# Optimization experiments

Hardware: AMD Instinct MI355X
Metric: run time of the kernel (lower is better)

## Reference

```python
import jax, jax.numpy as jnp
import numpy as np

DIM = 768
NUM_HEADS = 12
WH, WW = 14, 14
N_TOK = WH * WW + 1  # 197, includes CLS token
NUM_REL_DIST = (2 * WH - 1) * (2 * WW - 1) + 3  # 732
HEAD_DIM = DIM // NUM_HEADS
SCALE = HEAD_DIM ** -0.5


def _relative_position_index():
    # Mirrors the torch buffer construction (constant, int).
    coords = np.stack(np.meshgrid(np.arange(WH), np.arange(WW), indexing='ij'))  # [2,WH,WW]
    cf = coords.reshape(2, -1)  # [2, WH*WW]
    rel = cf[:, :, None] - cf[:, None, :]  # [2, N, N]
    rel = rel.transpose(1, 2, 0).astype(np.int64)
    rel[:, :, 0] += WH - 1
    rel[:, :, 1] += WW - 1
    rel[:, :, 0] *= 2 * WW - 1
    idx = np.zeros((N_TOK, N_TOK), dtype=np.int64)
    idx[1:, 1:] = rel.sum(-1)
    idx[0, 0:] = NUM_REL_DIST - 3
    idx[0:, 0] = NUM_REL_DIST - 2
    idx[0, 0] = NUM_REL_DIST - 1
    return jnp.asarray(idx)

REL_POS_INDEX = _relative_position_index()


def setup_inputs() -> dict:
    key = jax.random.key(0)
    ks = jax.random.split(key, 7)
    B = 64
    x = jax.random.normal(ks[0], (B, N_TOK, DIM), dtype=jnp.float32)
    qkv_weight = jax.random.normal(ks[1], (3 * DIM, DIM), dtype=jnp.float32) * 0.02
    q_bias = jax.random.normal(ks[2], (DIM,), dtype=jnp.float32) * 0.02
    v_bias = jax.random.normal(ks[3], (DIM,), dtype=jnp.float32) * 0.02
    rel_pos_bias_table = jax.random.normal(ks[4], (NUM_REL_DIST, NUM_HEADS), dtype=jnp.float32) * 0.02
    proj_weight = jax.random.normal(ks[5], (DIM, DIM), dtype=jnp.float32) * 0.02
    proj_bias = jax.random.normal(ks[6], (DIM,), dtype=jnp.float32) * 0.02
    return {"x": x, "qkv_weight": qkv_weight, "q_bias": q_bias, "v_bias": v_bias,
            "rel_pos_bias_table": rel_pos_bias_table, "proj_weight": proj_weight,
            "proj_bias": proj_bias}


def reference(x, qkv_weight, q_bias, v_bias, rel_pos_bias_table, proj_weight, proj_bias):
    B, N, C = x.shape
    qkv_bias = jnp.concatenate([q_bias, jnp.zeros_like(v_bias), v_bias])
    qkv = x @ qkv_weight.T + qkv_bias  # [B, N, 3C]
    qkv = qkv.reshape(B, N, 3, NUM_HEADS, HEAD_DIM).transpose(2, 0, 3, 1, 4)
    q, k, v = qkv[0], qkv[1], qkv[2]  # each [B, H, N, D]
    attn = jnp.einsum('bhnd,bhmd->bhnm', q * SCALE, k)  # [B, H, N, N]
    rpb = rel_pos_bias_table[REL_POS_INDEX]  # [N, N, H]
    attn = attn + rpb.transpose(2, 0, 1)[None]  # [1, H, N, N]
    attn = jax.nn.softmax(attn, axis=-1)
    out = jnp.einsum('bhnm,bhmd->bhnd', attn, v)  # [B, H, N, D]
    out = out.transpose(0, 2, 1, 3).reshape(B, N, C)
    return out @ proj_weight.T + proj_bias
```

## Files before the change

### kernel.cpp

```cpp
#include <hip/hip_runtime.h>
#include <hip/hip_bf16.h>

#define DIM 768
#define QKVD 2304
#define NHEADS 12
#define NTOK 197
#define NP 208
#define NPS 232
#define M_ROWS 12608
#define M_PAD 12800
#define HEADS_TOT 768
#define NT 24

typedef __attribute__((ext_vector_type(8))) short bf16x8;
typedef __attribute__((ext_vector_type(4))) float f32x4;

__device__ inline short f2bf(float f) {
  union { __hip_bfloat16 h; short s; } u;
  u.h = __float2bfloat16(f);
  return u.s;
}

__device__ __forceinline__ void gload16(const short* g, short* l) {
  __builtin_amdgcn_global_load_lds((const __attribute__((address_space(1))) void*)g,
                                   (__attribute__((address_space(3))) void*)l, 16, 0, 0);
}

__device__ __forceinline__ int xcd_swz(int orig, int nwg) {
  int q = nwg >> 3, r = nwg & 7;
  int x = orig & 7, p = orig >> 3;
  return (x < r ? x * (q + 1) : r * (q + 1) + (x - r) * q) + p;
}

__global__ void prep_kernel(const float* __restrict__ x, const float* __restrict__ wq,
                            const float* __restrict__ wp, const float* __restrict__ table,
                            short* __restrict__ xb, short* __restrict__ wqb,
                            short* __restrict__ wpb, float* __restrict__ rpbf) {
  int idx = blockIdx.x * 256 + threadIdx.x;
  const int n_x  = M_ROWS * DIM / 4;
  const int n_wq = 3 * DIM * DIM / 4;
  const int n_wp = DIM * DIM / 4;
  const int n_pad = (M_PAD - M_ROWS) * DIM / 4;
  const int conv_tot = n_x + n_wq + n_wp + n_pad;
  if (idx < conv_tot) {
    if (idx >= n_x + n_wq + n_wp) {
      int k = idx - n_x - n_wq - n_wp;
      short4 z = {0, 0, 0, 0};
      *(short4*)(xb + (size_t)M_ROWS * DIM + (size_t)k * 4) = z;
      return;
    }
    const float4* src; short* dst; int off;
    if (idx < n_x)             { src = (const float4*)x;  dst = xb;  off = idx; }
    else if (idx < n_x + n_wq) { src = (const float4*)wq; dst = wqb; off = idx - n_x; }
    else                       { src = (const float4*)wp; dst = wpb; off = idx - n_x - n_wq; }
    float4 v = src[off];
    short4 o;
    o.x = f2bf(v.x); o.y = f2bf(v.y); o.z = f2bf(v.z); o.w = f2bf(v.w);
    *(short4*)(dst + (size_t)off * 4) = o;
    return;
  }
  int ridx = idx - conv_tot;
  if (ridx >= NHEADS * NP * NP) return;
  int h = ridx / (NP * NP);
  int rem = ridx - h * NP * NP;
  int i = rem / NP;
  int j = rem - i * NP;
  float v = 0.f;
  if (i < NTOK && j < NTOK) {
    int t;
    if (i == 0 && j == 0) t = 731;
    else if (i == 0)      t = 729;
    else if (j == 0)      t = 730;
    else {
      int p = i - 1, q = j - 1;
      int ri = p / 14, ci = p - ri * 14;
      int rj = q / 14, cj = q - rj * 14;
      t = (ri - rj + 13) * 27 + (ci - cj + 13);
    }
    v = table[t * NHEADS + h];
  }
  rpbf[ridx] = v;
}

__device__ __forceinline__ void tile_step(int kt, short* lds,
                                          const short* Asrc, const short* Bsrc, short* sdst,
                                          int aoff, int boff,
                                          bf16x8 (&afc)[8], bf16x8 (&bfc)[4],
                                          bf16x8 (&afn)[8], bf16x8 (&bfn)[4],
                                          f32x4 (&acc)[8][4]) {
  const bool stg = (kt < NT - 3);
  const bool pre = (kt < NT - 1);
  const short* nb = lds + ((kt + 1) & 3) * 16384;
  short* stgd = sdst + ((kt + 3) & 3) * 16384;
  const int kc = (kt + 3) * 32;
  if (stg) { gload16(Asrc + kc, stgd); gload16(Bsrc + kc, stgd + 8192); }
  if (pre) {
#pragma unroll
    for (int n = 0; n < 4; ++n) bfn[n] = *(const bf16x8*)(nb + boff + n * 512);
#pragma unroll
    for (int j = 0; j < 4; ++j) afn[j] = *(const bf16x8*)(nb + aoff + j * 512);
  }
  __builtin_amdgcn_s_setprio(1);
#pragma unroll
  for (int j = 0; j < 4; ++j)
#pragma unroll
    for (int n = 0; n < 4; ++n)
      acc[j][n] = __builtin_amdgcn_mfma_f32_16x16x32_bf16(afc[j], bfc[n], acc[j][n], 0, 0, 0);
  __builtin_amdgcn_s_setprio(0);
  if (stg) { gload16(Asrc + (size_t)128 * DIM + kc, stgd + 4096);
             gload16(Bsrc + (size_t)128 * DIM + kc, stgd + 8192 + 4096); }
  if (pre) {
#pragma unroll
    for (int j = 0; j < 4; ++j) afn[4 + j] = *(const bf16x8*)(nb + aoff + 2048 + j * 512);
  }
  __builtin_amdgcn_s_setprio(1);
#pragma unroll
  for (int j = 0; j < 4; ++j)
#pragma unroll
    for (int n = 0; n < 4; ++n)
      acc[4 + j][n] = __builtin_amdgcn_mfma_f32_16x16x32_bf16(afc[4 + j], bfc[n], acc[4 + j][n], 0, 0, 0);
  __builtin_amdgcn_s_setprio(0);
  if (kt < NT - 3)       { asm volatile("s_waitcnt vmcnt(4)" ::: "memory"); }
  else if (kt == NT - 3) { asm volatile("s_waitcnt vmcnt(0)" ::: "memory"); }
  __builtin_amdgcn_s_barrier();
}

__device__ __forceinline__ void gemm256_mainloop(const short* __restrict__ A,
                                                 const short* __restrict__ Bw,
                                                 int tm, int tn, short* lds, f32x4 (&acc)[8][4]) {
  const int tid = threadIdx.x;
  const int srow = tid >> 2;
  const int sslot = ((tid & 3) - (tid >> 3)) & 3;
  const int l = tid & 63, lr = l & 15, lg = l >> 4;
  const int w = tid >> 6, wm = w >> 2, wn = w & 3;
  const short* Asrc = A + (size_t)(tm * 256 + srow) * DIM + sslot * 8;
  const short* Bsrc = Bw + (size_t)(tn * 256 + srow) * DIM + sslot * 8;
  short* sdst = lds + tid * 8;
  const int slotR = (lg + (lr >> 1)) & 3;
  const int aoff = wm * 4096 + lr * 32 + slotR * 8;
  const int boff = 8192 + (wn >> 1) * 4096 + ((wn & 1) * 64 + lr) * 32 + slotR * 8;
#pragma unroll
  for (int m = 0; m < 8; ++m)
#pragma unroll
    for (int n = 0; n < 4; ++n) { f32x4 z = {0.f, 0.f, 0.f, 0.f}; acc[m][n] = z; }

#pragma unroll
  for (int kt = 0; kt < 3; ++kt) {
    gload16(Asrc + kt * 32, sdst + kt * 16384);
    gload16(Bsrc + kt * 32, sdst + kt * 16384 + 8192);
    gload16(Asrc + (size_t)128 * DIM + kt * 32, sdst + kt * 16384 + 4096);
    gload16(Bsrc + (size_t)128 * DIM + kt * 32, sdst + kt * 16384 + 8192 + 4096);
  }
  asm volatile("s_waitcnt vmcnt(4)" ::: "memory");
  __builtin_amdgcn_s_barrier();

  bf16x8 afA[8], bfA[4], afB[8], bfB[4];
#pragma unroll
  for (int n = 0; n < 4; ++n) bfA[n] = *(const bf16x8*)(lds + boff + n * 512);
#pragma unroll
  for (int j = 0; j < 4; ++j) afA[j] = *(const bf16x8*)(lds + aoff + j * 512);
#pragma unroll
  for (int j = 0; j < 4; ++j) afA[4 + j] = *(const bf16x8*)(lds + aoff + 2048 + j * 512);

  for (int kt = 0; kt < NT; kt += 2) {
    tile_step(kt,     lds, Asrc, Bsrc, sdst, aoff, boff, afA, bfA, afB, bfB, acc);
    tile_step(kt + 1, lds, Asrc, Bsrc, sdst, aoff, boff, afB, bfB, afA, bfA, acc);
  }
}

__global__ __launch_bounds__(512, 2)
void gemm_qkv_kernel(const short* __restrict__ xb, const short* __restrict__ wqb,
                     const float* __restrict__ q_bias, const float* __restrict__ v_bias,
                     short* __restrict__ qkvb) {
  __shared__ __attribute__((aligned(16))) short lds[65536];
  const int wg = xcd_swz(blockIdx.x, 50 * 9);
  const int tn = wg % 9, tm = wg / 9;
  f32x4 acc[8][4];
  gemm256_mainloop(xb, wqb, tm, tn, lds, acc);

  const int tid = threadIdx.x;
  const int w = tid >> 6, wm = w >> 2, wn = w & 3;
  const int l = tid & 63, lr = l & 15, lg = l >> 4;
  const int cbase = tn * 256 + wn * 64;
  for (int half = 0; half < 2; ++half) {
    if (wm == half) {
#pragma unroll
      for (int n = 0; n < 4; ++n) {
        int c = cbase + n * 16 + lr;
        int part = (c < 768) ? 0 : ((c < 1536) ? 1 : 2);
        float bias = (part == 0) ? q_bias[c] : ((part == 2) ? v_bias[c - 1536] : 0.f);
        float scl = (part == 0) ? 0.125f : 1.f;
#pragma unroll
        for (int m = 0; m < 8; ++m)
#pragma unroll
          for (int i = 0; i < 4; ++i)
            lds[(m * 16 + lg * 4 + i) * 264 + wn * 64 + n * 16 + lr] =
                f2bf((acc[m][n][i] + bias) * scl);
      }
    }
    __syncthreads();
#pragma unroll
    for (int p = 0; p < 8; ++p) {
      int chunk = tid + p * 512;
      int row = chunk >> 5, ch = chunk & 31;
      bf16x8 v = *(const bf16x8*)(lds + row * 264 + ch * 8);
      *(bf16x8*)(qkvb + (size_t)(tm * 256 + half * 128 + row) * QKVD + tn * 256 + ch * 8) = v;
    }
    __syncthreads();
  }
}

__device__ __forceinline__ void tile_step128(int kt, short* lds,
                                             const short* Asrc, const short* Bsrc, short* sdst,
                                             int aoff, int boff,
                                             bf16x8 (&afc)[4], bf16x8 (&bfc)[4],
                                             bf16x8 (&afn)[4], bf16x8 (&bfn)[4],
                                             f32x4 (&acc)[4][4]) {
  const bool stg = (kt < NT - 3);
  const bool pre = (kt < NT - 1);
  const short* nb = lds + ((kt + 1) & 3) * 8192;
  short* stgd = sdst + ((kt + 3) & 3) * 8192;
  const int kc = (kt + 3) * 32;
  if (stg) { gload16(Asrc + kc, stgd); gload16(Bsrc + kc, stgd + 4096); }
  if (pre) {
#pragma unroll
    for (int n = 0; n < 4; ++n) bfn[n] = *(const bf16x8*)(nb + boff + n * 512);
#pragma unroll
    for (int j = 0; j < 2; ++j) afn[j] = *(const bf16x8*)(nb + aoff + j * 512);
  }
  __builtin_amdgcn_s_setprio(1);
#pragma unroll
  for (int j = 0; j < 2; ++j)
#pragma unroll
    for (int n = 0; n < 4; ++n)
      acc[j][n] = __builtin_amdgcn_mfma_f32_16x16x32_bf16(afc[j], bfc[n], acc[j][n], 0, 0, 0);
  __builtin_amdgcn_s_setprio(0);
  if (stg) { gload16(Asrc + (size_t)64 * DIM + kc, stgd + 2048);
             gload16(Bsrc + (size_t)64 * DIM + kc, stgd + 4096 + 2048); }
  if (pre) {
#pragma unroll
    for (int j = 2; j < 4; ++j) afn[j] = *(const bf16x8*)(nb + aoff + j * 512);
  }
  __builtin_amdgcn_s_setprio(1);
#pragma unroll
  for (int j = 2; j < 4; ++j)
#pragma unroll
    for (int n = 0; n < 4; ++n)
      acc[j][n] = __builtin_amdgcn_mfma_f32_16x16x32_bf16(afc[j], bfc[n], acc[j][n], 0, 0, 0);
  __builtin_amdgcn_s_setprio(0);
  if (kt < NT - 3)       { asm volatile("s_waitcnt vmcnt(4)" ::: "memory"); }
  else if (kt == NT - 3) { asm volatile("s_waitcnt vmcnt(0)" ::: "memory"); }
  __builtin_amdgcn_s_barrier();
}

__global__ __launch_bounds__(256, 2)
void gemm_proj_kernel(const short* __restrict__ ab, const short* __restrict__ wpb,
                      const float* __restrict__ proj_bias, float* __restrict__ out) {
  __shared__ __attribute__((aligned(16))) short lds[32768];
  const int wg = xcd_swz(blockIdx.x, 99 * 6);
  const int tn = wg % 6, tm = wg / 6;
  const int tid = threadIdx.x;
  const int srow = tid >> 2;
  const int sslot = ((tid & 3) - (tid >> 3)) & 3;
  const int l = tid & 63, lr = l & 15, lg = l >> 4;
  const int w = tid >> 6, wm = w >> 1, wn = w & 1;
  const short* Asrc = ab + (size_t)(tm * 128 + srow) * DIM + sslot * 8;
  const short* Bsrc = wpb + (size_t)(tn * 128 + srow) * DIM + sslot * 8;
  short* sdst = lds + tid * 8;
  const int slotR = (lg + (lr >> 1)) & 3;
  const int aoff = wm * 2048 + lr * 32 + slotR * 8;
  const int boff = 4096 + wn * 2048 + lr * 32 + slotR * 8;
  f32x4 acc[4][4];
#pragma unroll
  for (int m = 0; m < 4; ++m)
#pragma unroll
    for (int n = 0; n < 4; ++n) { f32x4 z = {0.f, 0.f, 0.f, 0.f}; acc[m][n] = z; }

#pragma unroll
  for (int kt = 0; kt < 3; ++kt) {
    gload16(Asrc + kt * 32, sdst + kt * 8192);
    gload16(Bsrc + kt * 32, sdst + kt * 8192 + 4096);
    gload16(Asrc + (size_t)64 * DIM + kt * 32, sdst + kt * 8192 + 2048);
    gload16(Bsrc + (size_t)64 * DIM + kt * 32, sdst + kt * 8192 + 4096 + 2048);
  }
  asm volatile("s_waitcnt vmcnt(4)" ::: "memory");
  __builtin_amdgcn_s_barrier();

  bf16x8 afA[4], bfA[4], afB[4], bfB[4];
#pragma unroll
  for (int n = 0; n < 4; ++n) bfA[n] = *(const bf16x8*)(lds + boff + n * 512);
#pragma unroll
  for (int j = 0; j < 4; ++j) afA[j] = *(const bf16x8*)(lds + aoff + j * 512);

  for (int kt = 0; kt < NT; kt += 2) {
    tile_step128(kt,     lds, Asrc, Bsrc, sdst, aoff, boff, afA, bfA, afB, bfB, acc);
    tile_step128(kt + 1, lds, Asrc, Bsrc, sdst, aoff, boff, afB, bfB, afA, bfA, acc);
  }

  float* ldsF = (float*)lds;
  for (int half = 0; half < 2; ++half) {
    if (wm == half) {
#pragma unroll
      for (int n = 0; n < 4; ++n) {
        int c = tn * 128 + wn * 64 + n * 16 + lr;
        float pb = proj_bias[c];
#pragma unroll
        for (int m = 0; m < 4; ++m)
#pragma unroll
          for (int i = 0; i < 4; ++i)
            ldsF[(m * 16 + lg * 4 + i) * 132 + wn * 64 + n * 16 + lr] = acc[m][n][i] + pb;
      }
    }
    __syncthreads();
#pragma unroll
    for (int p = 0; p < 8; ++p) {
      int chunk = tid + p * 256;
      int row = chunk >> 5, ch = chunk & 31;
      int r = tm * 128 + half * 64 + row;
      if (r < M_ROWS) {
        f32x4 v = *(const f32x4*)(ldsF + row * 132 + ch * 4);
        *(f32x4*)(out + (size_t)r * DIM + tn * 128 + ch * 4) = v;
      }
    }
    __syncthreads();
  }
}

__global__ __launch_bounds__(512, 1)
void attn_kernel(const short* __restrict__ qkvb, const float* __restrict__ rpbf,
                 short* __restrict__ aout) {
  __shared__ __attribute__((aligned(16))) short Klds[208 * 64];
  __shared__ __attribute__((aligned(16))) short Vlds[64 * NPS];
  __shared__ __attribute__((aligned(16))) short Plds[8 * 16 * NPS];
  const int bh = blockIdx.x;
  const int b = bh / 12, h = bh - b * 12;
  const short* base = qkvb + (size_t)(b * 197) * QKVD;
  const short* Qg = base + h * 64;
  const short* Kg = base + 768 + h * 64;
  const short* Vg = base + 1536 + h * 64;
  const float* RP = rpbf + (size_t)h * NP * NP;
  const int tid = threadIdx.x;
  const int wave = tid >> 6, l = tid & 63, lr = l & 15, lg = l >> 4;

  for (int c = tid; c < 1664; c += 512) {
    int r = c >> 3, sp = c & 7;
    int rr = r < NTOK ? r : NTOK - 1;
    gload16(Kg + (size_t)rr * QKVD + ((sp ^ (r & 7)) << 3), Klds + c * 8);
  }
  for (int idx = tid; idx < 64 * NP; idx += 512) {
    int t = idx >> 6, d = idx & 63;
    int tt = t < NTOK ? t : NTOK - 1;
    Vlds[d * NPS + t] = Vg[(size_t)tt * QKVD + d];
  }
  __syncthreads();
  if (tid < 64) {
    for (int j = NP; j < NPS; ++j) Vlds[tid * NPS + j] = 0;
  }
  __syncthreads();

  short* Pw = Plds + wave * 16 * NPS;
  for (int s = wave; s < 13; s += 8) {
    const int row0 = s * 16;
    const int qrow = (row0 + lr < NTOK) ? (row0 + lr) : (NTOK - 1);
    bf16x8 qf0 = *(const bf16x8*)(Qg + (size_t)qrow * QKVD + lg * 8);
    bf16x8 qf1 = *(const bf16x8*)(Qg + (size_t)qrow * QKVD + 32 + lg * 8);
    f32x4 acc[13];
#pragma unroll
    for (int t = 0; t < 13; ++t) { f32x4 z = {0.f, 0.f, 0.f, 0.f}; acc[t] = z; }
    __builtin_amdgcn_s_setprio(1);
#pragma unroll
    for (int t = 0; t < 13; ++t) {
      int rk = t * 16 + lr;
      int sw = lr & 7;
      bf16x8 kf0 = *(const bf16x8*)(Klds + rk * 64 + ((lg ^ sw) << 3));
      bf16x8 kf1 = *(const bf16x8*)(Klds + rk * 64 + (((4 + lg) ^ sw) << 3));
      acc[t] = __builtin_amdgcn_mfma_f32_16x16x32_bf16(qf0, kf0, acc[t], 0, 0, 0);
      acc[t] = __builtin_amdgcn_mfma_f32_16x16x32_bf16(qf1, kf1, acc[t], 0, 0, 0);
    }
    __builtin_amdgcn_s_setprio(0);
    float sum4[4];
#pragma unroll
    for (int i = 0; i < 4; ++i) {
      const int row = row0 + lg * 4 + i;
      const float* rp = RP + (size_t)row * NP;
      float sv[13];
      float mx = -3e38f;
#pragma unroll
      for (int t = 0; t < 13; ++t) {
        int col = t * 16 + lr;
        float s_ = (col < NTOK) ? (acc[t][i] + rp[col]) : -3e38f;
        sv[t] = s_;
        mx = fmaxf(mx, s_);
      }
      mx = fmaxf(mx, __shfl_xor(mx, 1, 16));
      mx = fmaxf(mx, __shfl_xor(mx, 2, 16));
      mx = fmaxf(mx, __shfl_xor(mx, 4, 16));
      mx = fmaxf(mx, __shfl_xor(mx, 8, 16));
      float sm = 0.f;
#pragma unroll
      for (int t = 0; t < 13; ++t) {
        float p = __expf(sv[t] - mx);
        sm += p;
        Pw[(lg * 4 + i) * NPS + t * 16 + lr] = f2bf(p);
      }
      sm += __shfl_xor(sm, 1, 16);
      sm += __shfl_xor(sm, 2, 16);
      sm += __shfl_xor(sm, 4, 16);
      sm += __shfl_xor(sm, 8, 16);
      sum4[i] = sm;
      Pw[(lg * 4 + i) * NPS + 208 + lr] = 0;
    }
    f32x4 o[4];
#pragma unroll
    for (int dt = 0; dt < 4; ++dt) { f32x4 z = {0.f, 0.f, 0.f, 0.f}; o[dt] = z; }
    __builtin_amdgcn_s_setprio(1);
#pragma unroll
    for (int jb = 0; jb < 7; ++jb) {
      bf16x8 pf = *(const bf16x8*)(Pw + lr * NPS + jb * 32 + lg * 8);
#pragma unroll
      for (int dt = 0; dt < 4; ++dt) {
        bf16x8 vf = *(const bf16x8*)(Vlds + (dt * 16 + lr) * NPS + jb * 32 + lg * 8);
        o[dt] = __builtin_amdgcn_mfma_f32_16x16x32_bf16(pf, vf, o[dt], 0, 0, 0);
      }
    }
    __builtin_amdgcn_s_setprio(0);
#pragma unroll
    for (int i = 0; i < 4; ++i) {
      const int row = row0 + lg * 4 + i;
      if (row < NTOK) {
        float inv = 1.f / sum4[i];
        size_t base2 = (size_t)(b * 197 + row) * DIM + h * 64;
#pragma unroll
        for (int dt = 0; dt < 4; ++dt)
          aout[base2 + dt * 16 + lr] = f2bf(o[dt][i] * inv);
      }
    }
  }
}

extern "C" void kernel_launch(void* const* d_in, const int* in_sizes, int n_in,
                              void* d_out, int out_size, void* d_ws, size_t ws_size,
                              hipStream_t stream) {
  const float* x         = (const float*)d_in[0];
  const float* wqkv      = (const float*)d_in[1];
  const float* q_bias    = (const float*)d_in[2];
  const float* v_bias    = (const float*)d_in[3];
  const float* table     = (const float*)d_in[4];
  const float* wproj     = (const float*)d_in[5];
  const float* proj_bias = (const float*)d_in[6];
  float* out = (float*)d_out;

  char* p = (char*)d_ws;
  short* xb    = (short*)p; p += (size_t)M_PAD * DIM * 2;
  short* wqb   = (short*)p; p += (size_t)3 * DIM * DIM * 2;
  short* wpb   = (short*)p; p += (size_t)DIM * DIM * 2;
  short* qkvb  = (short*)p; p += (size_t)M_PAD * QKVD * 2;
  float* rpbf  = (float*)p; p += (size_t)NHEADS * NP * NP * 4;
  short* aout  = xb;

  const int conv_tot = (M_ROWS * DIM + 3 * DIM * DIM + DIM * DIM + (M_PAD - M_ROWS) * DIM) / 4;
  const int prep_tot = conv_tot + NHEADS * NP * NP;
  prep_kernel<<<(prep_tot + 255) / 256, 256, 0, stream>>>(x, wqkv, wproj, table, xb, wqb, wpb, rpbf);
  gemm_qkv_kernel<<<50 * 9, 512, 0, stream>>>(xb, wqb, q_bias, v_bias, qkvb);
  attn_kernel<<<HEADS_TOT, 512, 0, stream>>>(qkvb, rpbf, aout);
  gemm_proj_kernel<<<99 * 6, 256, 0, stream>>>(aout, wpb, proj_bias, out);
}
```

Measured before the change: 141.6 us.

## Shrink attention blocks to 256 threads with two per CU and compact LDS

```diff
diff --git a/kernel.cpp b/kernel.cpp
--- a/kernel.cpp
+++ b/kernel.cpp
@@ -6,7 +6,8 @@
 #define NHEADS 12
 #define NTOK 197
 #define NP 208
-#define NPS 232
+#define VST 208
+#define PST 216
 #define M_ROWS 12608
 #define M_PAD 12800
 #define HEADS_TOT 768
@@ -326,12 +327,12 @@
   }
 }
 
-__global__ __launch_bounds__(512, 1)
+__global__ __launch_bounds__(256, 2)
 void attn_kernel(const short* __restrict__ qkvb, const float* __restrict__ rpbf,
                  short* __restrict__ aout) {
   __shared__ __attribute__((aligned(16))) short Klds[208 * 64];
-  __shared__ __attribute__((aligned(16))) short Vlds[64 * NPS];
-  __shared__ __attribute__((aligned(16))) short Plds[8 * 16 * NPS];
+  __shared__ __attribute__((aligned(16))) short Vlds[64 * VST];
+  __shared__ __attribute__((aligned(16))) short Plds[4 * 16 * PST];
   const int bh = blockIdx.x;
   const int b = bh / 12, h = bh - b * 12;
   const short* base = qkvb + (size_t)(b * 197) * QKVD;
@@ -342,24 +343,24 @@
   const int tid = threadIdx.x;
   const int wave = tid >> 6, l = tid & 63, lr = l & 15, lg = l >> 4;
 
-  for (int c = tid; c < 1664; c += 512) {
+  for (int c = tid; c < 1664; c += 256) {
     int r = c >> 3, sp = c & 7;
     int rr = r < NTOK ? r : NTOK - 1;
     gload16(Kg + (size_t)rr * QKVD + ((sp ^ (r & 7)) << 3), Klds + c * 8);
   }
-  for (int idx = tid; idx < 64 * NP; idx += 512) {
-    int t = idx >> 6, d = idx & 63;
+  for (int vi = tid; vi < 1664; vi += 256) {
+    int t = vi >> 3, j = vi & 7;
     int tt = t < NTOK ? t : NTOK - 1;
-    Vlds[d * NPS + t] = Vg[(size_t)tt * QKVD + d];
+    bf16x8 v = *(const bf16x8*)(Vg + (size_t)tt * QKVD + j * 8);
+    int ts = t ^ ((j & 1) << 3);
+#pragma unroll
+    for (int e = 0; e < 8; ++e)
+      Vlds[(j * 8 + e) * VST + ts] = v[e];
   }
   __syncthreads();
-  if (tid < 64) {
-    for (int j = NP; j < NPS; ++j) Vlds[tid * NPS + j] = 0;
-  }
-  __syncthreads();
-
-  short* Pw = Plds + wave * 16 * NPS;
-  for (int s = wave; s < 13; s += 8) {
+
+  short* Pw = Plds + wave * 16 * PST;
+  for (int s = wave; s < 13; s += 4) {
     const int row0 = s * 16;
     const int qrow = (row0 + lr < NTOK) ? (row0 + lr) : (NTOK - 1);
     bf16x8 qf0 = *(const bf16x8*)(Qg + (size_t)qrow * QKVD + lg * 8);
@@ -401,26 +402,37 @@
       for (int t = 0; t < 13; ++t) {
         float p = __expf(sv[t] - mx);
         sm += p;
-        Pw[(lg * 4 + i) * NPS + t * 16 + lr] = f2bf(p);
+        Pw[(lg * 4 + i) * PST + t * 16 + lr] = f2bf(p);
       }
       sm += __shfl_xor(sm, 1, 16);
       sm += __shfl_xor(sm, 2, 16);
       sm += __shfl_xor(sm, 4, 16);
       sm += __shfl_xor(sm, 8, 16);
       sum4[i] = sm;
-      Pw[(lg * 4 + i) * NPS + 208 + lr] = 0;
     }
     f32x4 o[4];
 #pragma unroll
     for (int dt = 0; dt < 4; ++dt) { f32x4 z = {0.f, 0.f, 0.f, 0.f}; o[dt] = z; }
+    const int vswz = ((lr >> 3) & 1) << 3;
     __builtin_amdgcn_s_setprio(1);
 #pragma unroll
-    for (int jb = 0; jb < 7; ++jb) {
-      bf16x8 pf = *(const bf16x8*)(Pw + lr * NPS + jb * 32 + lg * 8);
+    for (int jb = 0; jb < 6; ++jb) {
+      bf16x8 pf = *(const bf16x8*)(Pw + lr * PST + jb * 32 + lg * 8);
 #pragma unroll
       for (int dt = 0; dt < 4; ++dt) {
-        bf16x8 vf = *(const bf16x8*)(Vlds + (dt * 16 + lr) * NPS + jb * 32 + lg * 8);
+        bf16x8 vf = *(const bf16x8*)(Vlds + (dt * 16 + lr) * VST + ((jb * 32 + lg * 8) ^ vswz));
         o[dt] = __builtin_amdgcn_mfma_f32_16x16x32_bf16(pf, vf, o[dt], 0, 0, 0);
+      }
+    }
+    {
+      bf16x8 zf = {0, 0, 0, 0, 0, 0, 0, 0};
+      bf16x8 pf6 = zf;
+      if (lg < 2) pf6 = *(const bf16x8*)(Pw + lr * PST + 192 + lg * 8);
+#pragma unroll
+      for (int dt = 0; dt < 4; ++dt) {
+        bf16x8 vf6 = zf;
+        if (lg < 2) vf6 = *(const bf16x8*)(Vlds + (dt * 16 + lr) * VST + ((192 + lg * 8) ^ vswz));
+        o[dt] = __builtin_amdgcn_mfma_f32_16x16x32_bf16(pf6, vf6, o[dt], 0, 0, 0);
       }
     }
     __builtin_amdgcn_s_setprio(0);
@@ -462,6 +474,6 @@
   const int prep_tot = conv_tot + NHEADS * NP * NP;
   prep_kernel<<<(prep_tot + 255) / 256, 256, 0, stream>>>(x, wqkv, wproj, table, xb, wqb, wpb, rpbf);
   gemm_qkv_kernel<<<50 * 9, 512, 0, stream>>>(xb, wqb, q_bias, v_bias, qkvb);
-  attn_kernel<<<HEADS_TOT, 512, 0, stream>>>(qkvb, rpbf, aout);
+  attn_kernel<<<HEADS_TOT, 256, 0, stream>>>(qkvb, rpbf, aout);
   gemm_proj_kernel<<<99 * 6, 256, 0, stream>>>(aout, wpb, proj_bias, out);
 }
```

Result: slower. 147.2 us (+3.9%).
